# Kernel optimization log

Hardware: AMD Instinct MI355X
Metric: run time of the kernel (lower is better)

## Reference

```python
import jax, jax.numpy as jnp
import numpy as np
import math


def setup_inputs() -> dict:
    key = jax.random.key(0)
    ks = jax.random.split(key, 8)
    B, C, H, W = 8, 512, 48, 48
    Cq = C // 8
    s = 0.05
    return {
        "x": jax.random.normal(ks[0], (B, C, H, W), jnp.float32),
        "Wq": jax.random.normal(ks[1], (Cq, C), jnp.float32) * s,
        "bq": jax.random.normal(ks[2], (Cq,), jnp.float32) * s,
        "Wk": jax.random.normal(ks[3], (Cq, C), jnp.float32) * s,
        "bk": jax.random.normal(ks[4], (Cq,), jnp.float32) * s,
        "Wv": jax.random.normal(ks[5], (C, C), jnp.float32) * s,
        "bv": jax.random.normal(ks[6], (C,), jnp.float32) * s,
        "gamma": jax.random.normal(ks[7], (1,), jnp.float32),
    }


def reference(x, Wq, bq, Wk, bk, Wv, bv, gamma):
    B, C, H, W = x.shape
    Cq = Wq.shape[0]
    N = H * W
    xf = x.reshape(B, C, N)  # 1x1 conv == channel matmul
    q = jnp.einsum('oc,bcn->bno', Wq, xf) + bq  # [B, N, Cq] (proj_query, permuted)
    k = jnp.einsum('oc,bcn->bon', Wk, xf) + bk[None, :, None]  # [B, Cq, N]
    v = jnp.einsum('oc,bcn->bon', Wv, xf) + bv[None, :, None]  # [B, C, N]
    # ave_I = (1/Cq)*(I - (1/Cq)*J); Q @ ave_I = (Q - rowmean(Q)) / Cq
    qc = (q - jnp.mean(q, axis=-1, keepdims=True)) / Cq
    sigma = jnp.einsum('bnc,bcm->bnm', qc, k) / math.sqrt(Cq)  # [B, N, N]
    attention = jax.nn.softmax(sigma, axis=-1)
    # out = V @ attention^T : out[b,c,n] = sum_m v[b,c,m] * attention[b,n,m]
    am = jnp.einsum('bcm,bnm->bcn', v, attention).reshape(B, C, H, W)
    out = gamma[0] * am + x
    return out
```

## Files before the change

kernel.cpp:

```cpp
#include <hip/hip_runtime.h>

#define B_ 8
#define C_ 512
#define N_ 2304
#define CQ 64

typedef float f32x4 __attribute__((ext_vector_type(4)));
typedef float f32x16 __attribute__((ext_vector_type(16)));
typedef short bf16x8 __attribute__((ext_vector_type(8)));
typedef unsigned short u16x4 __attribute__((ext_vector_type(4)));
typedef unsigned short u16x8 __attribute__((ext_vector_type(8)));
typedef int i32x4 __attribute__((ext_vector_type(4)));

__device__ __forceinline__ unsigned short f2bf(float f){
  union { float f; unsigned int u; } v; v.f = f;
  unsigned int r = (v.u + 0x7fffu + ((v.u >> 16) & 1u)) >> 16;
  return (unsigned short)r;
}

__device__ __forceinline__ void gload_lds16(const void* g, void* l){
  __builtin_amdgcn_global_load_lds(
      (const __attribute__((address_space(1))) unsigned int*)g,
      (__attribute__((address_space(3))) unsigned int*)l, 16, 0, 0);
}

__global__ __launch_bounds__(256) void k_wcvt(const float* __restrict__ Wq,
                                              const float* __restrict__ Wk,
                                              const float* __restrict__ Wv,
                                              unsigned short* __restrict__ Wb){
  int idx = blockIdx.x*256 + threadIdx.x;
  int h = idx & 1, ln = (idx >> 1) & 31, cs = (idx >> 6) & 31, ob = idx >> 11;
  int row = ob*32 + ln, col = cs*16 + h*8;
  const float* src;
  if (row < 64)       src = Wq + (size_t)row*512 + col;
  else if (row < 128) src = Wk + (size_t)(row-64)*512 + col;
  else                src = Wv + (size_t)(row-128)*512 + col;
  f32x4 v0 = *(const f32x4*)src;
  f32x4 v1 = *(const f32x4*)(src + 4);
  u16x8 o;
  #pragma unroll
  for (int j = 0; j < 4; j++){ o[j] = f2bf(v0[j]); o[4+j] = f2bf(v1[j]); }
  *(u16x8*)(Wb + (size_t)idx*8) = o;
}

__global__ __launch_bounds__(512) void k_prep(const float* __restrict__ x,
                                              const float* __restrict__ bq,
                                              const float* __restrict__ bk,
                                              const float* __restrict__ bv,
                                              const unsigned short* __restrict__ Wb,
                                              unsigned short* __restrict__ qw,
                                              unsigned short* __restrict__ kw,
                                              unsigned short* __restrict__ vw){
  __shared__ short xt_l[32*520];
  __shared__ float scr[2*32*68];

  int i = blockIdx.x; int b = i & 7; int nt = i >> 3;
  int n0 = nt*32;
  int t = threadIdx.x; int w = t >> 6; int l = t & 63;
  int h = l >> 5, ln = l & 31;
  const size_t bN = (size_t)b*N_;

  #pragma unroll
  for (int it = 0; it < 8; it++){
    int c = it*64 + (t >> 3);
    int n4 = (t & 7)*4;
    f32x4 v = *(const f32x4*)(x + ((size_t)b*C_ + c)*N_ + n0 + n4);
    #pragma unroll
    for (int j = 0; j < 4; j++) xt_l[(n4+j)*520 + c] = (short)f2bf(v[j]);
  }
  __syncthreads();

  const unsigned short* wlane = Wb + (size_t)(ln*2 + h)*8;
  const unsigned short* wv0 = wlane + (size_t)(4 + 2*w)*16384;
  const unsigned short* wv1 = wlane + (size_t)(5 + 2*w)*16384;
  const unsigned short* wqk = wlane + (size_t)w*16384;

  f32x16 vacc[2]; f32x16 qkacc;
  #pragma unroll
  for (int rr = 0; rr < 16; rr++){ vacc[0][rr]=0.f; vacc[1][rr]=0.f; qkacc[rr]=0.f; }

  #pragma unroll 8
  for (int cs = 0; cs < 32; cs++){
    bf16x8 bx = *(const bf16x8*)&xt_l[ln*520 + cs*16 + h*8];
    bf16x8 a0 = *(const bf16x8*)(wv0 + (size_t)cs*512);
    bf16x8 a1 = *(const bf16x8*)(wv1 + (size_t)cs*512);
    vacc[0] = __builtin_amdgcn_mfma_f32_32x32x16_bf16(a0, bx, vacc[0], 0, 0, 0);
    vacc[1] = __builtin_amdgcn_mfma_f32_32x32x16_bf16(a1, bx, vacc[1], 0, 0, 0);
    if (w < 4){
      bf16x8 aq = *(const bf16x8*)(wqk + (size_t)cs*512);
      qkacc = __builtin_amdgcn_mfma_f32_32x32x16_bf16(aq, bx, qkacc, 0, 0, 0);
    }
  }

  if (w < 4){
    float* s = scr + ((w >> 1) ? 2176 : 0);
    int obase = (w & 1)*32;
    #pragma unroll
    for (int rr = 0; rr < 16; rr++){
      int o = obase + (rr & 3) + 8*(rr >> 2) + 4*h;
      s[ln*68 + o] = qkacc[rr];
    }
  }
  __syncthreads();

  if (t < 256){
    int isK = t >> 7;
    int tt = t & 127;
    int n = tt >> 2, j = tt & 3;
    const float* s = scr + (isK ? 2176 : 0);
    const float* bias = isK ? bk : bq;
    float vals[16]; float sm = 0.f;
    #pragma unroll
    for (int ii = 0; ii < 16; ii++){
      vals[ii] = s[n*68 + j*16 + ii] + bias[j*16 + ii];
      sm += vals[ii];
    }
    sm += __shfl_xor(sm, 1); sm += __shfl_xor(sm, 2);
    float mean = isK ? 0.f : sm * (1.f/64.f);
    float scl  = isK ? 1.f : (1.44269504089f/512.f);
    u16x8 h0, h1;
    #pragma unroll
    for (int ii = 0; ii < 8; ii++) h0[ii] = f2bf((vals[ii]   - mean)*scl);
    #pragma unroll
    for (int ii = 0; ii < 8; ii++) h1[ii] = f2bf((vals[8+ii] - mean)*scl);
    unsigned short* d = (isK ? kw : qw) + (bN + n0 + n)*CQ + j*16;
    *(u16x8*)d = h0;
    *(u16x8*)(d + 8) = h1;
  }
  __syncthreads();

  #pragma unroll
  for (int r = 0; r < 4; r++){
    if ((w >> 1) == r){
      float* s = scr + (w & 1)*2176;
      #pragma unroll
      for (int of = 0; of < 2; of++)
        #pragma unroll
        for (int rr = 0; rr < 16; rr++){
          int o = of*32 + (rr & 3) + 8*(rr >> 2) + 4*h;
          s[ln*68 + o] = vacc[of][rr];
        }
    }
    __syncthreads();
    {
      int ch = t >> 8;
      int tt = t & 255;
      int o = tt >> 2, jj = (tt >> 1) & 1, half = tt & 1;
      int og = (2*r + ch)*64 + o;
      const float* s = scr + ch*2176;
      float bvv = bv[og];
      u16x8 hv;
      #pragma unroll
      for (int ii = 0; ii < 8; ii++){
        int q2 = ((ii & 3) | ((ii & 4) << 1)) + half*4;
        hv[ii] = f2bf(s[(jj*16 + q2)*68 + o] + bvv);
      }
      *(u16x8*)(vw + ((size_t)b*C_ + og)*N_ + n0 + jj*16 + half*8) = hv;
    }
    __syncthreads();
  }
}

__global__ __launch_bounds__(256) void k_sexp(const unsigned short* __restrict__ qw,
                                              const unsigned short* __restrict__ kw,
                                              unsigned short* __restrict__ Pl,
                                              float* __restrict__ lsum_part,
                                              int b0, int bsh){
  int bid = blockIdx.x;
  int bl = bid & ((1 << bsh) - 1);
  int b = b0 + bl;
  int r = bid >> bsh;
  int ms = r & 3; int nt = r >> 2;
  int t = threadIdx.x; int w = t >> 6; int l = t & 63;
  int h = l >> 5, ln = l & 31;
  int nf = w & 1, mh = w >> 1;
  int n = nt*64 + nf*32 + ln;

  const unsigned short* qb = qw + ((size_t)b*N_ + n)*CQ + h*8;
  bf16x8 qf[4];
  #pragma unroll
  for (int kq = 0; kq < 4; kq++) qf[kq] = *(const bf16x8*)(qb + kq*16);

  int mb32base = ms*18 + mh*9;
  const unsigned short* ks0 = kw + ((size_t)b*N_ + ln)*CQ + h*8 + (size_t)mb32base*32*CQ;
  unsigned short* pb = Pl + ((size_t)bl*144*N_ + n)*16 + h*8;

  float lsum = 0.f;
  bf16x8 ka[4], kc[4];
  #pragma unroll
  for (int kq = 0; kq < 4; kq++) ka[kq] = *(const bf16x8*)(ks0 + kq*16);

  #define SEXP_BODY(MF, KF, KN, PFOFF)                                          \
  {                                                                             \
    _Pragma("unroll")                                                           \
    for (int kq = 0; kq < 4; kq++)                                              \
      KN[kq] = *(const bf16x8*)(ks0 + (size_t)(PFOFF)*32*CQ + kq*16);           \
    f32x16 sv;                                                                  \
    _Pragma("unroll")                                                           \
    for (int rr = 0; rr < 16; rr++) sv[rr] = 0.f;                               \
    _Pragma("unroll")                                                           \
    for (int kq = 0; kq < 4; kq++)                                              \
      sv = __builtin_amdgcn_mfma_f32_32x32x16_bf16(KF[kq], qf[kq], sv, 0, 0, 0);\
    float e[16];                                                                \
    _Pragma("unroll")                                                           \
    for (int rr = 0; rr < 16; rr++) e[rr] = exp2f(sv[rr]);                      \
    _Pragma("unroll")                                                           \
    for (int rr = 0; rr < 16; rr++) lsum += e[rr];                              \
    unsigned int pd[8];                                                         \
    _Pragma("unroll")                                                           \
    for (int j = 0; j < 8; j++)                                                 \
      asm("v_cvt_pk_bf16_f32 %0, %1, %2" : "=v"(pd[j]) : "v"(e[2*j]), "v"(e[2*j+1])); \
    i32x4 lo = (i32x4){(int)pd[0],(int)pd[1],(int)pd[2],(int)pd[3]};            \
    i32x4 hi = (i32x4){(int)pd[4],(int)pd[5],(int)pd[6],(int)pd[7]};            \
    unsigned short* d = pb + (size_t)((mb32base + (MF))*2)*N_*16;               \
    *(i32x4*)d = lo;                                                            \
    *(i32x4*)(d + (size_t)N_*16) = hi;                                          \
  }

  #pragma unroll
  for (int it = 0; it < 4; it++){
    SEXP_BODY(2*it,     ka, kc, 2*it + 1)
    SEXP_BODY(2*it + 1, kc, ka, 2*it + 2)
  }
  SEXP_BODY(8, ka, kc, 8)
  #undef SEXP_BODY

  lsum += __shfl_xor(lsum, 32);
  if (l < 32)
    lsum_part[((size_t)bl*8 + ms*2 + mh)*N_ + n] = lsum;
}

__global__ __launch_bounds__(256, 1) void k_pv(const unsigned short* __restrict__ vw,
                                               const unsigned short* __restrict__ Pl,
                                               const float* __restrict__ lsum_part,
                                               const float* __restrict__ x,
                                               const float* __restrict__ gamma_p,
                                               float* __restrict__ out,
                                               int b0, int bsh){
  __shared__ __attribute__((aligned(16))) short At[3][128*64];

  int bid = blockIdx.x;
  int bl = bid & ((1 << bsh) - 1);
  int b = b0 + bl;
  int r = bid >> bsh;
  int cb = r & 3; int nb = r >> 2;
  int c0 = cb*128, n0g = nb*64;
  int t = threadIdx.x; int w = t >> 6; int l = t & 63;
  int h = l >> 5, ln = l & 31;
  int wc = w & 1, wn = w >> 1;

  int gc = ((l & 7) - (l >> 3)) & 7;
  const unsigned short* asrc0 = vw + ((size_t)b*C_ + c0 + w*32 + (l >> 3))*N_ + gc*8;
  int aro[2][4];
  #pragma unroll
  for (int cf = 0; cf < 2; cf++)
    #pragma unroll
    for (int mb = 0; mb < 4; mb++){
      int row = wc*64 + cf*32 + ln;
      aro[cf][mb] = (row*8 + ((mb*2 + h + row) & 7)) * 16;
    }
  const unsigned short* Pb = Pl + (size_t)bl*144*N_*16;
  size_t bstep = (size_t)N_*16;
  int boff = (n0g + wn*32 + ln)*16 + h*8;

  f32x16 acc[2];
  #pragma unroll
  for (int cf = 0; cf < 2; cf++)
    #pragma unroll
    for (int rr = 0; rr < 16; rr++) acc[cf][rr] = 0.f;

  bf16x8 B0[4], B1[4], B2[4];

  #pragma unroll
  for (int j = 0; j < 4; j++)
    gload_lds16(asrc0 + (size_t)j*8*N_, &At[0][w*2048 + j*512]);
  #pragma unroll
  for (int mb = 0; mb < 4; mb++)
    B0[mb] = *(const bf16x8*)(Pb + (size_t)mb*bstep + boff);
  #pragma unroll
  for (int j = 0; j < 4; j++)
    gload_lds16(asrc0 + (size_t)j*8*N_ + 64, &At[1][w*2048 + j*512]);
  #pragma unroll
  for (int mb = 0; mb < 4; mb++)
    B1[mb] = *(const bf16x8*)(Pb + (size_t)(4 + mb)*bstep + boff);
  asm volatile("s_waitcnt vmcnt(12)" ::: "memory");
  __builtin_amdgcn_s_barrier();
  __builtin_amdgcn_sched_barrier(0);

  #define PV_STEP(KT, RD, WR, BC, BN)                                           \
  {                                                                             \
    const char* Ab = (const char*)At[RD];                                       \
    bf16x8 a_[2][4];                                                            \
    _Pragma("unroll")                                                           \
    for (int cf = 0; cf < 2; cf++)                                              \
      _Pragma("unroll")                                                         \
      for (int mb = 0; mb < 4; mb++)                                            \
        a_[cf][mb] = *(const bf16x8*)(Ab + aro[cf][mb]);                        \
    int m2 = ((KT) + 2 < 36) ? ((KT) + 2)*64 : 0;                               \
    _Pragma("unroll")                                                           \
    for (int j = 0; j < 4; j++)                                                 \
      gload_lds16(asrc0 + (size_t)j*8*N_ + m2, &At[WR][w*2048 + j*512]);        \
    {                                                                           \
      size_t mb2 = (size_t)((((KT) + 2 < 36) ? ((KT) + 2)*4 : 0));              \
      _Pragma("unroll")                                                         \
      for (int mb = 0; mb < 4; mb++)                                            \
        BN[mb] = *(const bf16x8*)(Pb + (mb2 + mb)*bstep + boff);                \
    }                                                                           \
    _Pragma("unroll")                                                           \
    for (int cf = 0; cf < 2; cf++)                                              \
      _Pragma("unroll")                                                         \
      for (int mb = 0; mb < 4; mb++)                                            \
        acc[cf] = __builtin_amdgcn_mfma_f32_32x32x16_bf16(                      \
            a_[cf][mb], BC[mb], acc[cf], 0, 0, 0);                              \
    asm volatile("s_waitcnt vmcnt(12) lgkmcnt(0)" ::: "memory");                \
    __builtin_amdgcn_s_barrier();                                               \
    __builtin_amdgcn_sched_barrier(0);                                          \
  }

  for (int it = 0; it < 6; it++){
    int kt = it*6;
    PV_STEP(kt+0, 0, 2, B0, B2)
    PV_STEP(kt+1, 1, 0, B1, B0)
    PV_STEP(kt+2, 2, 1, B2, B1)
    PV_STEP(kt+3, 0, 2, B0, B2)
    PV_STEP(kt+4, 1, 0, B1, B0)
    PV_STEP(kt+5, 2, 1, B2, B1)
  }
  #undef PV_STEP

  float gmv = gamma_p[0];
  {
    int n = n0g + wn*32 + ln;
    float s = 0.f;
    #pragma unroll
    for (int j = 0; j < 8; j++) s += lsum_part[((size_t)bl*8 + j)*N_ + n];
    float f = gmv / s;
    #pragma unroll
    for (int cf = 0; cf < 2; cf++){
      #pragma unroll
      for (int rr = 0; rr < 16; rr++){
        int c = c0 + wc*64 + cf*32 + (rr & 3) + 8*(rr >> 2) + 4*h;
        size_t idx = ((size_t)b*C_ + c)*N_ + n;
        out[idx] = acc[cf][rr]*f + x[idx];
      }
    }
  }
}

extern "C" void kernel_launch(void* const* d_in, const int* in_sizes, int n_in,
                              void* d_out, int out_size, void* d_ws, size_t ws_size,
                              hipStream_t stream) {
  (void)in_sizes; (void)n_in; (void)out_size;
  const float* x  = (const float*)d_in[0];
  const float* Wq = (const float*)d_in[1];
  const float* bq = (const float*)d_in[2];
  const float* Wk = (const float*)d_in[3];
  const float* bk = (const float*)d_in[4];
  const float* Wv = (const float*)d_in[5];
  const float* bv = (const float*)d_in[6];
  const float* gm = (const float*)d_in[7];
  float* out = (float*)d_out;

  const size_t qw_b = (size_t)B_*N_*CQ*2;
  const size_t vw_b = (size_t)B_*C_*N_*2;
  const size_t wb_b = (size_t)640*512*2;

  int nbg = 8, bsh = 3;
  for (;;){
    size_t pl_b   = (size_t)nbg*144*N_*16*2;
    size_t lsum_b = (size_t)nbg*8*N_*4;
    size_t need   = pl_b + 2*qw_b + vw_b + lsum_b + wb_b;
    if (need <= ws_size || nbg == 1) break;
    nbg >>= 1; bsh--;
  }
  size_t pl_b   = (size_t)nbg*144*N_*16*2;
  size_t lsum_b = (size_t)nbg*8*N_*4;

  char* wsc = (char*)d_ws;
  unsigned short* Pl = (unsigned short*)wsc;
  unsigned short* qw = (unsigned short*)(wsc + pl_b);
  unsigned short* kw = (unsigned short*)(wsc + pl_b + qw_b);
  unsigned short* vw = (unsigned short*)(wsc + pl_b + 2*qw_b);
  float* lsum_part   = (float*)(wsc + pl_b + 2*qw_b + vw_b);
  unsigned short* Wb = (unsigned short*)(wsc + pl_b + 2*qw_b + vw_b + lsum_b);

  k_wcvt<<<160, 256, 0, stream>>>(Wq, Wk, Wv, Wb);
  k_prep<<<576, 512, 0, stream>>>(x, bq, bk, bv, Wb, qw, kw, vw);

  for (int b0 = 0; b0 < B_; b0 += nbg){
    k_sexp<<<144*nbg, 256, 0, stream>>>(qw, kw, Pl, lsum_part, b0, bsh);
    k_pv<<<144*nbg, 256, 0, stream>>>(vw, Pl, lsum_part, x, gm, out, b0, bsh);
  }
}
```

Baseline: 128.8 us.

## Store V in MFMA fragment layout and load A operands directly to registers

The prep kernel now writes V in a blocked layout that matches the MFMA A-fragment order, so the PV kernel can load A operands straight from global memory into registers with double buffering. This drops the LDS staging buffers, the global-to-LDS loads and the per-step workgroup barriers, and adds s_setprio around the MFMA block. The cost is more live registers and more global load instructions per wave. Removing the LDS allocation and the launch_bounds min-blocks hint may also allow higher occupancy.

```diff
diff --git a/kernel.cpp b/kernel.cpp
--- a/kernel.cpp
+++ b/kernel.cpp
@@ -16,12 +16,6 @@
   union { float f; unsigned int u; } v; v.f = f;
   unsigned int r = (v.u + 0x7fffu + ((v.u >> 16) & 1u)) >> 16;
   return (unsigned short)r;
-}
-
-__device__ __forceinline__ void gload_lds16(const void* g, void* l){
-  __builtin_amdgcn_global_load_lds(
-      (const __attribute__((address_space(1))) unsigned int*)g,
-      (__attribute__((address_space(3))) unsigned int*)l, 16, 0, 0);
 }
 
 __global__ __launch_bounds__(256) void k_wcvt(const float* __restrict__ Wq,
@@ -50,7 +44,7 @@
                                               const unsigned short* __restrict__ Wb,
                                               unsigned short* __restrict__ qw,
                                               unsigned short* __restrict__ kw,
-                                              unsigned short* __restrict__ vw){
+                                              unsigned short* __restrict__ vb){
   __shared__ short xt_l[32*520];
   __shared__ float scr[2*32*68];
 
@@ -155,7 +149,8 @@
         int q2 = ((ii & 3) | ((ii & 4) << 1)) + half*4;
         hv[ii] = f2bf(s[(jj*16 + q2)*68 + o] + bvv);
       }
-      *(u16x8*)(vw + ((size_t)b*C_ + og)*N_ + n0 + jj*16 + half*8) = hv;
+      size_t dst = (((size_t)b*144 + 2*nt + jj)*16 + (og >> 5))*512 + (og & 31)*16 + half*8;
+      *(u16x8*)(vb + dst) = hv;
     }
     __syncthreads();
   }
@@ -230,15 +225,13 @@
     lsum_part[((size_t)bl*8 + ms*2 + mh)*N_ + n] = lsum;
 }
 
-__global__ __launch_bounds__(256, 1) void k_pv(const unsigned short* __restrict__ vw,
-                                               const unsigned short* __restrict__ Pl,
-                                               const float* __restrict__ lsum_part,
-                                               const float* __restrict__ x,
-                                               const float* __restrict__ gamma_p,
-                                               float* __restrict__ out,
-                                               int b0, int bsh){
-  __shared__ __attribute__((aligned(16))) short At[3][128*64];
-
+__global__ __launch_bounds__(256) void k_pv(const unsigned short* __restrict__ vb,
+                                            const unsigned short* __restrict__ Pl,
+                                            const float* __restrict__ lsum_part,
+                                            const float* __restrict__ x,
+                                            const float* __restrict__ gamma_p,
+                                            float* __restrict__ out,
+                                            int b0, int bsh){
   int bid = blockIdx.x;
   int bl = bid & ((1 << bsh) - 1);
   int b = b0 + bl;
@@ -249,16 +242,12 @@
   int h = l >> 5, ln = l & 31;
   int wc = w & 1, wn = w >> 1;
 
-  int gc = ((l & 7) - (l >> 3)) & 7;
-  const unsigned short* asrc0 = vw + ((size_t)b*C_ + c0 + w*32 + (l >> 3))*N_ + gc*8;
-  int aro[2][4];
-  #pragma unroll
-  for (int cf = 0; cf < 2; cf++)
-    #pragma unroll
-    for (int mb = 0; mb < 4; mb++){
-      int row = wc*64 + cf*32 + ln;
-      aro[cf][mb] = (row*8 + ((mb*2 + h + row) & 7)) * 16;
-    }
+  const unsigned short* abase[2];
+  #pragma unroll
+  for (int cf = 0; cf < 2; cf++){
+    int cg = cb*4 + wc*2 + cf;
+    abase[cf] = vb + ((size_t)b*144*16 + cg)*512 + (ln*2 + h)*8;
+  }
   const unsigned short* Pb = Pl + (size_t)bl*144*N_*16;
   size_t bstep = (size_t)N_*16;
   int boff = (n0g + wn*32 + ln)*16 + h*8;
@@ -269,62 +258,57 @@
     #pragma unroll
     for (int rr = 0; rr < 16; rr++) acc[cf][rr] = 0.f;
 
+  bf16x8 A0[2][4], A1[2][4];
   bf16x8 B0[4], B1[4], B2[4];
 
   #pragma unroll
-  for (int j = 0; j < 4; j++)
-    gload_lds16(asrc0 + (size_t)j*8*N_, &At[0][w*2048 + j*512]);
+  for (int cf = 0; cf < 2; cf++)
+    #pragma unroll
+    for (int mb = 0; mb < 4; mb++)
+      A0[cf][mb] = *(const bf16x8*)(abase[cf] + (size_t)mb*8192);
   #pragma unroll
   for (int mb = 0; mb < 4; mb++)
     B0[mb] = *(const bf16x8*)(Pb + (size_t)mb*bstep + boff);
   #pragma unroll
-  for (int j = 0; j < 4; j++)
-    gload_lds16(asrc0 + (size_t)j*8*N_ + 64, &At[1][w*2048 + j*512]);
-  #pragma unroll
   for (int mb = 0; mb < 4; mb++)
     B1[mb] = *(const bf16x8*)(Pb + (size_t)(4 + mb)*bstep + boff);
-  asm volatile("s_waitcnt vmcnt(12)" ::: "memory");
-  __builtin_amdgcn_s_barrier();
+  asm volatile("s_waitcnt vmcnt(4)" ::: "memory");
   __builtin_amdgcn_sched_barrier(0);
 
-  #define PV_STEP(KT, RD, WR, BC, BN)                                           \
+  #define PV_STEP(KT, AC, AN, BC, BN)                                           \
   {                                                                             \
-    const char* Ab = (const char*)At[RD];                                       \
-    bf16x8 a_[2][4];                                                            \
+    int m1 = ((KT) + 1 < 36) ? ((KT) + 1)*4 : 0;                                \
     _Pragma("unroll")                                                           \
     for (int cf = 0; cf < 2; cf++)                                              \
       _Pragma("unroll")                                                         \
       for (int mb = 0; mb < 4; mb++)                                            \
-        a_[cf][mb] = *(const bf16x8*)(Ab + aro[cf][mb]);                        \
-    int m2 = ((KT) + 2 < 36) ? ((KT) + 2)*64 : 0;                               \
-    _Pragma("unroll")                                                           \
-    for (int j = 0; j < 4; j++)                                                 \
-      gload_lds16(asrc0 + (size_t)j*8*N_ + m2, &At[WR][w*2048 + j*512]);        \
+        AN[cf][mb] = *(const bf16x8*)(abase[cf] + (size_t)(m1 + mb)*8192);      \
     {                                                                           \
       size_t mb2 = (size_t)((((KT) + 2 < 36) ? ((KT) + 2)*4 : 0));              \
       _Pragma("unroll")                                                         \
       for (int mb = 0; mb < 4; mb++)                                            \
         BN[mb] = *(const bf16x8*)(Pb + (mb2 + mb)*bstep + boff);                \
     }                                                                           \
+    asm volatile("s_waitcnt vmcnt(12)" ::: "memory");                           \
+    __builtin_amdgcn_sched_barrier(0);                                          \
+    __builtin_amdgcn_s_setprio(1);                                              \
     _Pragma("unroll")                                                           \
     for (int cf = 0; cf < 2; cf++)                                              \
       _Pragma("unroll")                                                         \
       for (int mb = 0; mb < 4; mb++)                                            \
         acc[cf] = __builtin_amdgcn_mfma_f32_32x32x16_bf16(                      \
-            a_[cf][mb], BC[mb], acc[cf], 0, 0, 0);                              \
-    asm volatile("s_waitcnt vmcnt(12) lgkmcnt(0)" ::: "memory");                \
-    __builtin_amdgcn_s_barrier();                                               \
-    __builtin_amdgcn_sched_barrier(0);                                          \
+            AC[cf][mb], BC[mb], acc[cf], 0, 0, 0);                              \
+    __builtin_amdgcn_s_setprio(0);                                              \
   }
 
   for (int it = 0; it < 6; it++){
     int kt = it*6;
-    PV_STEP(kt+0, 0, 2, B0, B2)
-    PV_STEP(kt+1, 1, 0, B1, B0)
-    PV_STEP(kt+2, 2, 1, B2, B1)
-    PV_STEP(kt+3, 0, 2, B0, B2)
-    PV_STEP(kt+4, 1, 0, B1, B0)
-    PV_STEP(kt+5, 2, 1, B2, B1)
+    PV_STEP(kt+0, A0, A1, B0, B2)
+    PV_STEP(kt+1, A1, A0, B1, B0)
+    PV_STEP(kt+2, A0, A1, B2, B1)
+    PV_STEP(kt+3, A1, A0, B0, B2)
+    PV_STEP(kt+4, A0, A1, B1, B0)
+    PV_STEP(kt+5, A1, A0, B2, B1)
   }
   #undef PV_STEP
 
@@ -362,14 +346,14 @@
   float* out = (float*)d_out;
 
   const size_t qw_b = (size_t)B_*N_*CQ*2;
-  const size_t vw_b = (size_t)B_*C_*N_*2;
+  const size_t vb_b = (size_t)B_*144*16*512*2;
   const size_t wb_b = (size_t)640*512*2;
 
   int nbg = 8, bsh = 3;
   for (;;){
     size_t pl_b   = (size_t)nbg*144*N_*16*2;
     size_t lsum_b = (size_t)nbg*8*N_*4;
-    size_t need   = pl_b + 2*qw_b + vw_b + lsum_b + wb_b;
+    size_t need   = pl_b + 2*qw_b + vb_b + lsum_b + wb_b;
     if (need <= ws_size || nbg == 1) break;
     nbg >>= 1; bsh--;
   }
@@ -380,15 +364,15 @@
   unsigned short* Pl = (unsigned short*)wsc;
   unsigned short* qw = (unsigned short*)(wsc + pl_b);
   unsigned short* kw = (unsigned short*)(wsc + pl_b + qw_b);
-  unsigned short* vw = (unsigned short*)(wsc + pl_b + 2*qw_b);
-  float* lsum_part   = (float*)(wsc + pl_b + 2*qw_b + vw_b);
-  unsigned short* Wb = (unsigned short*)(wsc + pl_b + 2*qw_b + vw_b + lsum_b);
+  unsigned short* vb = (unsigned short*)(wsc + pl_b + 2*qw_b);
+  float* lsum_part   = (float*)(wsc + pl_b + 2*qw_b + vb_b);
+  unsigned short* Wb = (unsigned short*)(wsc + pl_b + 2*qw_b + vb_b + lsum_b);
 
   k_wcvt<<<160, 256, 0, stream>>>(Wq, Wk, Wv, Wb);
-  k_prep<<<576, 512, 0, stream>>>(x, bq, bk, bv, Wb, qw, kw, vw);
+  k_prep<<<576, 512, 0, stream>>>(x, bq, bk, bv, Wb, qw, kw, vb);
 
   for (int b0 = 0; b0 < B_; b0 += nbg){
     k_sexp<<<144*nbg, 256, 0, stream>>>(qw, kw, Pl, lsum_part, b0, bsh);
-    k_pv<<<144*nbg, 256, 0, stream>>>(vw, Pl, lsum_part, x, gm, out, b0, bsh);
-  }
-}
+    k_pv<<<144*nbg, 256, 0, stream>>>(vb, Pl, lsum_part, x, gm, out, b0, bsh);
+  }
+}
```

Result: slower. 151.5 us (+17.5%).
